# Performance work log

Hardware: AMD Instinct MI355X
Metric: run time of the kernel (lower is better)

Reference implementation:

```python
import jax, jax.numpy as jnp
import numpy as np

H_DIM = 256
N_HEADS = 8
HEAD_DIM = H_DIM // N_HEADS
B, N = 2, 2048
LN_EPS = 1e-5


def setup_inputs() -> dict:
    key = jax.random.key(0)
    ks = jax.random.split(key, 20)
    s = 1.0 / np.sqrt(H_DIM)
    inp = {
        'hidden': jax.random.normal(ks[0], (B, N, H_DIM), jnp.float32),
        'adjacency': jax.random.uniform(ks[1], (B, N, N), jnp.float32),
        'positions': jax.random.uniform(ks[2], (B, N, 2), jnp.float32),
        # linear weights stored as (in, out): y = x @ W + b
        'wq': jax.random.normal(ks[3], (H_DIM, H_DIM), jnp.float32) * s,
        'bq': jnp.zeros((H_DIM,), jnp.float32),
        'wk': jax.random.normal(ks[4], (H_DIM, H_DIM), jnp.float32) * s,
        'bk': jnp.zeros((H_DIM,), jnp.float32),
        'wv': jax.random.normal(ks[5], (H_DIM, H_DIM), jnp.float32) * s,
        'bv': jnp.zeros((H_DIM,), jnp.float32),
        'wo': jax.random.normal(ks[6], (H_DIM, H_DIM), jnp.float32) * s,
        'bo': jnp.zeros((H_DIM,), jnp.float32),
        'g1': jnp.ones((H_DIM,), jnp.float32),
        'b1': jnp.zeros((H_DIM,), jnp.float32),
        'g2': jnp.ones((H_DIM,), jnp.float32),
        'b2': jnp.zeros((H_DIM,), jnp.float32),
        'w_ff1': jax.random.normal(ks[7], (H_DIM, 4 * H_DIM), jnp.float32) * s,
        'b_ff1': jnp.zeros((4 * H_DIM,), jnp.float32),
        'w_ff2': jax.random.normal(ks[8], (4 * H_DIM, H_DIM), jnp.float32) * (1.0 / np.sqrt(4 * H_DIM)),
        'b_ff2': jnp.zeros((H_DIM,), jnp.float32),
    }
    return inp


def _layernorm(x, g, b):
    mu = jnp.mean(x, axis=-1, keepdims=True)
    var = jnp.var(x, axis=-1, keepdims=True)
    return (x - mu) * jax.lax.rsqrt(var + LN_EPS) * g + b


def reference(hidden, adjacency, positions, wq, bq, wk, bk, wv, bv, wo, bo,
              g1, b1, g2, b2, w_ff1, b_ff1, w_ff2, b_ff2):
    b_, n_, _ = hidden.shape
    normalized = _layernorm(hidden, g1, b1)
    # project and split heads: [B, H, N, Dh]
    def heads(x):
        return x.reshape(b_, n_, N_HEADS, HEAD_DIM).transpose(0, 2, 1, 3)
    q = heads(normalized @ wq + bq)
    k = heads(normalized @ wk + bk)
    v = heads(normalized @ wv + bv)
    logits = jnp.einsum('bhnd,bhmd->bhnm', q, k) / np.sqrt(HEAD_DIM)
    cond = adjacency[:, None, :, :]  # mode == 'connectivity'
    logits = logits + (2.0 * cond - 1.0)
    weights = jax.nn.softmax(logits, axis=-1)
    weights = weights * (0.25 + 0.75 * cond)
    weights = weights / jnp.maximum(weights.sum(axis=-1, keepdims=True), 1e-6)
    attended = jnp.einsum('bhnm,bhmd->bhnd', weights, v)
    attended = attended.transpose(0, 2, 1, 3).reshape(b_, n_, H_DIM)
    hidden = hidden + attended @ wo + bo
    h2 = _layernorm(hidden, g2, b2)
    ff = jax.nn.gelu(h2 @ w_ff1 + b_ff1, approximate=False) @ w_ff2 + b_ff2
    return hidden + ff
```

## Files before the change

### kernel.cpp

```cpp
#include <hip/hip_runtime.h>
#include <math.h>

#define BB 2
#define NN 2048
#define HD 256
#define NH 8
#define DH 32
#define NTOK (BB*NN)
#define QKVLD 768
#define NSPLIT 4

typedef _Float16 h8 __attribute__((ext_vector_type(8)));
typedef _Float16 h4 __attribute__((ext_vector_type(4)));
typedef float fx4 __attribute__((ext_vector_type(4)));

#define LOG2E 1.4426950408889634f
#define SQ_LOG2 0.25503486f

__global__ __launch_bounds__(256) void ln_kernel(const float* __restrict__ x,
    const float* __restrict__ g, const float* __restrict__ bta,
    _Float16* __restrict__ yh)
{
  int row  = blockIdx.x * 4 + (threadIdx.x >> 6);
  int lane = threadIdx.x & 63;
  const float* xr = x + (size_t)row * HD + lane * 4;
  float4 v = *(const float4*)xr;
  float s = v.x + v.y + v.z + v.w;
  #pragma unroll
  for (int off = 32; off > 0; off >>= 1) s += __shfl_xor(s, off);
  float mu = s * (1.0f / HD);
  float dx0 = v.x - mu, dx1 = v.y - mu, dx2 = v.z - mu, dx3 = v.w - mu;
  float ss = dx0*dx0 + dx1*dx1 + dx2*dx2 + dx3*dx3;
  #pragma unroll
  for (int off = 32; off > 0; off >>= 1) ss += __shfl_xor(ss, off);
  float rinv = rsqrtf(ss * (1.0f / HD) + 1e-5f);
  float4 gv = *(const float4*)(g   + lane * 4);
  float4 bv = *(const float4*)(bta + lane * 4);
  float o[4];
  o[0] = dx0 * rinv * gv.x + bv.x;
  o[1] = dx1 * rinv * gv.y + bv.y;
  o[2] = dx2 * rinv * gv.z + bv.z;
  o[3] = dx3 * rinv * gv.w + bv.w;
  h4 hh;
  #pragma unroll
  for (int j = 0; j < 4; j++) hh[j] = (_Float16)o[j];
  *(h4*)(yh + (size_t)row * HD + lane * 4) = hh;
}

__device__ __forceinline__ void do_transpose(const float* __restrict__ W,
    _Float16* __restrict__ Wh, int Nw, int rowoff, int ldout, float scale,
    int bx, int by, float (*tile)[33])
{
  int k0 = by * 32, n0 = bx * 32;
  int c = threadIdx.x & 31, r = threadIdx.x >> 5;
  #pragma unroll
  for (int i = 0; i < 4; i++)
    tile[r + i * 8][c] = W[(size_t)(k0 + r + i * 8) * Nw + n0 + c];
  __syncthreads();
  #pragma unroll
  for (int i = 0; i < 4; i++) {
    int n = r + i * 8;
    Wh[(size_t)(rowoff + n0 + n) * ldout + k0 + c] = (_Float16)(tile[c][n] * scale);
  }
}

__global__ __launch_bounds__(256) void prep_kernel(
    const float* wq, const float* wk, const float* wv, const float* wo,
    const float* wf1, const float* wf2,
    const float* bq, const float* bk, const float* bv,
    _Float16* WtQKVh, _Float16* WtOh, _Float16* WtF1h, _Float16* WtF2h,
    float* biasqkv)
{
  __shared__ float tile[32][33];
  int bid = blockIdx.x;
  if (bid < 64)        do_transpose(wq,  WtQKVh,  256,   0,  256, SQ_LOG2, bid & 7, bid >> 3, tile);
  else if (bid < 128)  do_transpose(wk,  WtQKVh,  256, 256,  256, 1.0f, (bid-64) & 7, (bid-64) >> 3, tile);
  else if (bid < 192)  do_transpose(wv,  WtQKVh,  256, 512,  256, 1.0f, (bid-128) & 7, (bid-128) >> 3, tile);
  else if (bid < 256)  do_transpose(wo,  WtOh,    256,   0,  256, 1.0f, (bid-192) & 7, (bid-192) >> 3, tile);
  else if (bid < 512)  do_transpose(wf1, WtF1h,  1024,   0,  256, 1.0f, (bid-256) & 31, (bid-256) >> 5, tile);
  else if (bid < 768)  do_transpose(wf2, WtF2h,   256,   0, 1024, 1.0f, (bid-512) & 7, (bid-512) >> 3, tile);
  else {
    #pragma unroll
    for (int j = 0; j < 3; j++) {
      int t = j * 256 + threadIdx.x;
      biasqkv[t] = (t < 256) ? bq[t] * SQ_LOG2 : (t < 512) ? bk[t - 256] : bv[t - 512];
    }
  }
}

template<int KK, int NT, int NX, int ACT, int RES, int OM>
__global__ __launch_bounds__(256) void gemm16_kernel(
    const _Float16* __restrict__ Ah, const _Float16* __restrict__ Wh,
    const float* __restrict__ bias, const float* __restrict__ resid,
    float* __restrict__ Cf, _Float16* __restrict__ Ch,
    _Float16* __restrict__ vtb, int N)
{
  const int lin = blockIdx.x;
  const int qch = gridDim.x >> 3;
  const int wg = (lin & 7) * qch + (lin >> 3);
  const int bx = wg % NX, by = wg / NX;
  const int n0 = bx * (NT * 16);
  const int m0 = by * 64;
  const int t = threadIdx.x, w = t >> 6, l = t & 63;
  const int ml = l & 15, g = l >> 4;
  const int mrow = m0 + w * 16 + ml;

  const _Float16* aph = Ah + (size_t)mrow * KK + g * 8;
  const _Float16* whp[NT];
  #pragma unroll
  for (int nt = 0; nt < NT; nt++)
    whp[nt] = Wh + (size_t)(n0 + nt * 16 + ml) * KK + g * 8;

  fx4 acc[NT];
  #pragma unroll
  for (int nt = 0; nt < NT; nt++) acc[nt] = (fx4){0.f, 0.f, 0.f, 0.f};

  #pragma unroll 4
  for (int k0 = 0; k0 < KK; k0 += 32) {
    h8 ah = *(const h8*)(aph + k0);
    #pragma unroll
    for (int nt = 0; nt < NT; nt++) {
      h8 wh = *(const h8*)(whp[nt] + k0);
      acc[nt] = __builtin_amdgcn_mfma_f32_16x16x32_f16(ah, wh, acc[nt], 0, 0, 0);
    }
  }

  #pragma unroll
  for (int nt = 0; nt < NT; nt++) {
    int n = n0 + nt * 16 + ml;
    float bv = bias[n];
    #pragma unroll
    for (int i = 0; i < 4; i++) {
      int m = m0 + w * 16 + 4 * g + i;
      float vv = acc[nt][i] + bv;
      if (ACT == 1) vv = 0.5f * vv * (1.0f + erff(vv * 0.70710678118654752f));
      if (RES)      vv += resid[(size_t)m * N + n];
      if (OM == 0) {
        Cf[(size_t)m * N + n] = vv;
      } else if (OM == 1) {
        Ch[(size_t)m * N + n] = (_Float16)vv;
      } else {
        if (n < 512) Ch[(size_t)m * QKVLD + n] = (_Float16)vv;
        else {
          int dim = n - 512, kv = m & (NN - 1), bb = m >> 11;
          int kvp = (kv & ~31) | ((kv & 15) << 1) | ((kv >> 4) & 1);
          vtb[((size_t)(bb * HD + dim)) * NN + kvp] = (_Float16)vv;
        }
      }
    }
  }
}

__global__ __launch_bounds__(256) void attn_mfma_kernel(
    const _Float16* __restrict__ qkv16, const _Float16* __restrict__ vtb,
    const float* __restrict__ adj,
    float* __restrict__ Opart, float* __restrict__ Mpart, float* __restrict__ Spart)
{
  __shared__ _Float16 Ksh[64][40];
  __shared__ _Float16 Vp[32][72];

  const int z = blockIdx.z;
  const int b = z >> 2, quarter = z & 3;
  const int h = blockIdx.y;
  const int q0 = blockIdx.x * 64;
  const int t = threadIdx.x;
  const int w = t >> 6, l = t & 63;
  const int m = l & 15, g = l >> 4;
  const int kvbase = quarter * (NN / NSPLIT);

  const int qrow = q0 + w * 16 + m;
  h8 qh = *(const h8*)(qkv16 + ((size_t)(b * NN + qrow)) * QKVLD + h * DH + g * 8);

  fx4 ot0 = {0.f, 0.f, 0.f, 0.f};
  fx4 ot1 = {0.f, 0.f, 0.f, 0.f};
  float M = -3.0e38f, S = 0.0f;

  const float* adjrow = adj + ((size_t)(b * NN + qrow)) * NN + kvbase;

  const int krow = t >> 2, kd0 = (t & 3) * 8;
  const int vdim = t >> 3, vkc = (t & 7) * 8;
  const _Float16* kbase = qkv16 + ((size_t)(b * NN + kvbase + krow)) * QKVLD + 256 + h * DH + kd0;
  const _Float16* vbase = vtb + ((size_t)(b * HD + h * DH + vdim)) * NN + kvbase + vkc;
  h8 kreg = *(const h8*)kbase;
  h8 vreg = *(const h8*)vbase;
  float4 adjreg[4];
  #pragma unroll
  for (int p = 0; p < 4; p++) adjreg[p] = *(const float4*)(adjrow + p * 16 + g * 4);

  for (int kt = 0; kt < NN / NSPLIT; kt += 64) {
    __syncthreads();
    *(h8*)&Ksh[krow][kd0] = kreg;
    *(h8*)&Vp[vdim][vkc]  = vreg;
    __syncthreads();

    float4 a4[4];
    #pragma unroll
    for (int p = 0; p < 4; p++) a4[p] = adjreg[p];
    if (kt + 64 < NN / NSPLIT) {
      kreg = *(const h8*)(kbase + (size_t)(kt + 64) * QKVLD);
      vreg = *(const h8*)(vbase + kt + 64);
      #pragma unroll
      for (int p = 0; p < 4; p++) adjreg[p] = *(const float4*)(adjrow + kt + 64 + p * 16 + g * 4);
    }

    h8 kh0 = *(const h8*)&Ksh[     m][g * 8];
    h8 kh1 = *(const h8*)&Ksh[16 + m][g * 8];
    h8 kh2 = *(const h8*)&Ksh[32 + m][g * 8];
    h8 kh3 = *(const h8*)&Ksh[48 + m][g * 8];
    fx4 z4 = {0.f, 0.f, 0.f, 0.f};
    fx4 st[4];
    st[0] = __builtin_amdgcn_mfma_f32_16x16x32_f16(kh0, qh, z4, 0, 0, 0);
    st[1] = __builtin_amdgcn_mfma_f32_16x16x32_f16(kh1, qh, z4, 0, 0, 0);
    st[2] = __builtin_amdgcn_mfma_f32_16x16x32_f16(kh2, qh, z4, 0, 0, 0);
    st[3] = __builtin_amdgcn_mfma_f32_16x16x32_f16(kh3, qh, z4, 0, 0, 0);

    float lv[16];
    float tmax = -3.0e38f;
    #pragma unroll
    for (int p = 0; p < 4; p++) {
      const float* ap = (const float*)&a4[p];
      #pragma unroll
      for (int i = 0; i < 4; i++) {
        float lvv = st[p][i] + (2.0f * LOG2E) * ap[i] - LOG2E;
        lv[p * 4 + i] = lvv;
        tmax = fmaxf(tmax, lvv);
      }
    }
    tmax = fmaxf(tmax, __shfl_xor(tmax, 16));
    tmax = fmaxf(tmax, __shfl_xor(tmax, 32));
    if (!__all(tmax <= M + 8.0f)) {
      float mnew = fmaxf(M, tmax);
      float resc = __builtin_amdgcn_exp2f(M - mnew);
      S *= resc; ot0 *= resc; ot1 *= resc;
      M = mnew;
    }
    float pv[16];
    #pragma unroll
    for (int p = 0; p < 4; p++) {
      const float* ap = (const float*)&a4[p];
      #pragma unroll
      for (int i = 0; i < 4; i++) {
        float e = __builtin_amdgcn_exp2f(lv[p * 4 + i] - M);
        float pp = (0.25f + 0.75f * ap[i]) * e;
        pv[p * 4 + i] = pp;
        S += pp;
      }
    }
    h8 ph0, ph1;
    #pragma unroll
    for (int q2 = 0; q2 < 4; q2++) {
      ph0[2*q2]     = (_Float16)pv[q2];
      ph0[2*q2 + 1] = (_Float16)pv[4 + q2];
      ph1[2*q2]     = (_Float16)pv[8 + q2];
      ph1[2*q2 + 1] = (_Float16)pv[12 + q2];
    }

    h8 v00 = *(const h8*)&Vp[m][g * 8];
    h8 v01 = *(const h8*)&Vp[m][32 + g * 8];
    h8 v10 = *(const h8*)&Vp[16 + m][g * 8];
    h8 v11 = *(const h8*)&Vp[16 + m][32 + g * 8];
    ot0 = __builtin_amdgcn_mfma_f32_16x16x32_f16(v00, ph0, ot0, 0, 0, 0);
    ot0 = __builtin_amdgcn_mfma_f32_16x16x32_f16(v01, ph1, ot0, 0, 0, 0);
    ot1 = __builtin_amdgcn_mfma_f32_16x16x32_f16(v10, ph0, ot1, 0, 0, 0);
    ot1 = __builtin_amdgcn_mfma_f32_16x16x32_f16(v11, ph1, ot1, 0, 0, 0);
  }

  S += __shfl_xor(S, 16);
  S += __shfl_xor(S, 32);

  size_t prow = ((size_t)(z * NH + h)) * NN + qrow;
  float* po = Opart + prow * 32;
  *(float4*)(po + 4 * g)      = make_float4(ot0[0], ot0[1], ot0[2], ot0[3]);
  *(float4*)(po + 16 + 4 * g) = make_float4(ot1[0], ot1[1], ot1[2], ot1[3]);
  if (g == 0) { Mpart[prow] = M; Spart[prow] = S; }
}

__global__ __launch_bounds__(256) void attn_combine_kernel(
    const float* __restrict__ Opart, const float* __restrict__ Mpart,
    const float* __restrict__ Spart, _Float16* __restrict__ atth)
{
  int idx = blockIdx.x * 256 + threadIdx.x;
  int dg  = idx & 7;
  int rowid = idx >> 3;
  int qrow = rowid & (NN - 1);
  int bh = rowid >> 11;
  int b = bh >> 3, h = bh & 7;
  size_t p[NSPLIT];
  float mz[NSPLIT], sz[NSPLIT];
  float mm = -3.0e38f;
  #pragma unroll
  for (int zq = 0; zq < NSPLIT; zq++) {
    p[zq] = ((size_t)((b * NSPLIT + zq) * NH + h)) * NN + qrow;
    mz[zq] = Mpart[p[zq]];
    sz[zq] = Spart[p[zq]];
    mm = fmaxf(mm, mz[zq]);
  }
  float den = 0.f;
  float ez[NSPLIT];
  #pragma unroll
  for (int zq = 0; zq < NSPLIT; zq++) {
    ez[zq] = __builtin_amdgcn_exp2f(mz[zq] - mm);
    den += sz[zq] * ez[zq];
  }
  float is = 1.0f / den;
  float ov[4] = {0.f, 0.f, 0.f, 0.f};
  #pragma unroll
  for (int zq = 0; zq < NSPLIT; zq++) {
    float4 o = *(const float4*)(Opart + p[zq] * 32 + dg * 4);
    ov[0] += o.x * ez[zq]; ov[1] += o.y * ez[zq];
    ov[2] += o.z * ez[zq]; ov[3] += o.w * ez[zq];
  }
  h4 hh;
  #pragma unroll
  for (int j = 0; j < 4; j++) hh[j] = (_Float16)(ov[j] * is);
  *(h4*)(atth + ((size_t)(b * NN + qrow)) * HD + h * DH + dg * 4) = hh;
}

extern "C" void kernel_launch(void* const* d_in, const int* in_sizes, int n_in,
                              void* d_out, int out_size, void* d_ws, size_t ws_size,
                              hipStream_t stream)
{
  const float* hidden    = (const float*)d_in[0];
  const float* adjacency = (const float*)d_in[1];
  const float* wq  = (const float*)d_in[3];
  const float* bq  = (const float*)d_in[4];
  const float* wk  = (const float*)d_in[5];
  const float* bk  = (const float*)d_in[6];
  const float* wv  = (const float*)d_in[7];
  const float* bv  = (const float*)d_in[8];
  const float* wo  = (const float*)d_in[9];
  const float* bo  = (const float*)d_in[10];
  const float* g1  = (const float*)d_in[11];
  const float* b1  = (const float*)d_in[12];
  const float* g2  = (const float*)d_in[13];
  const float* b2  = (const float*)d_in[14];
  const float* wf1 = (const float*)d_in[15];
  const float* bf1 = (const float*)d_in[16];
  const float* wf2 = (const float*)d_in[17];
  const float* bf2 = (const float*)d_in[18];
  float* out = (float*)d_out;

  char* base = (char*)d_ws;
  const size_t MB = 1024 * 1024;
  _Float16* norm1h = (_Float16*)(base);
  _Float16* qkv16  = (_Float16*)(base + 4*MB);
  _Float16* vtb    = (_Float16*)(base + 10*MB);
  _Float16* atth   = (_Float16*)(base + 12*MB);
  float*    hid2   = (float*)(base + 16*MB);
  float* Opart = (float*)(base + 20*MB);
  _Float16* ffah = (_Float16*)(base + 20*MB);
  float* Mpart = (float*)(base + 36*MB);
  float* Spart = (float*)(base + 36*MB + 512*1024);
  _Float16* wtb = (_Float16*)(base + 37*MB);
  _Float16* WtQKVh = wtb; wtb += 768 * 256;
  _Float16* WtOh   = wtb; wtb += 256 * 256;
  _Float16* WtF1h  = wtb; wtb += 1024 * 256;
  _Float16* WtF2h  = wtb; wtb += 256 * 1024;
  float* biasqkv = (float*)(base + 40*MB);

  prep_kernel<<<769, 256, 0, stream>>>(wq, wk, wv, wo, wf1, wf2, bq, bk, bv,
      WtQKVh, WtOh, WtF1h, WtF2h, biasqkv);

  ln_kernel<<<NTOK / 4, 256, 0, stream>>>(hidden, g1, b1, norm1h);

  gemm16_kernel<256, 4, 12, 0, 0, 2><<<768, 256, 0, stream>>>(
      norm1h, WtQKVh, biasqkv, nullptr, nullptr, qkv16, vtb, QKVLD);

  attn_mfma_kernel<<<dim3(NN / 64, NH, BB * NSPLIT), 256, 0, stream>>>(
      qkv16, vtb, adjacency, Opart, Mpart, Spart);
  attn_combine_kernel<<<(BB * NH * NN * 8) / 256, 256, 0, stream>>>(
      Opart, Mpart, Spart, atth);

  gemm16_kernel<256, 2, 8, 0, 1, 0><<<512, 256, 0, stream>>>(
      atth, WtOh, bo, hidden, hid2, nullptr, nullptr, 256);

  ln_kernel<<<NTOK / 4, 256, 0, stream>>>(hid2, g2, b2, norm1h);

  gemm16_kernel<256, 4, 16, 1, 0, 1><<<1024, 256, 0, stream>>>(
      norm1h, WtF1h, bf1, nullptr, nullptr, ffah, nullptr, 1024);

  gemm16_kernel<1024, 2, 8, 0, 1, 0><<<512, 256, 0, stream>>>(
      ffah, WtF2h, bf2, hid2, out, nullptr, nullptr, 256);
}
```

Measured before the change: 133.4 us.

## Double-buffer attention K/V tiles and store normalized fp16 partial outputs

The attention kernel now keeps two LDS buffers for K and V and writes the next tile after the current tile's MFMAs, so each iteration needs one barrier instead of two. The row-max reduction is restructured to shuffle only when a rescale is needed. Each split's partial output is normalized by its own sum and stored as fp16, which halves partial-output traffic, and the combine kernel reweights by S·exp. This adds LDS use and a small fp16 precision loss on the partials.

After: 132.0 us. Within noise of the previous version (-1.0%).

```diff
diff --git a/kernel.cpp b/kernel.cpp
--- a/kernel.cpp
+++ b/kernel.cpp
@@ -154,10 +154,10 @@
 __global__ __launch_bounds__(256) void attn_mfma_kernel(
     const _Float16* __restrict__ qkv16, const _Float16* __restrict__ vtb,
     const float* __restrict__ adj,
-    float* __restrict__ Opart, float* __restrict__ Mpart, float* __restrict__ Spart)
-{
-  __shared__ _Float16 Ksh[64][40];
-  __shared__ _Float16 Vp[32][72];
+    _Float16* __restrict__ Opart, float* __restrict__ Mpart, float* __restrict__ Spart)
+{
+  __shared__ _Float16 Ksh[2][64][40];
+  __shared__ _Float16 Vp[2][32][72];
 
   const int z = blockIdx.z;
   const int b = z >> 2, quarter = z & 3;
@@ -167,6 +167,7 @@
   const int w = t >> 6, l = t & 63;
   const int m = l & 15, g = l >> 4;
   const int kvbase = quarter * (NN / NSPLIT);
+  const int NTILES = NN / NSPLIT / 64;
 
   const int qrow = q0 + w * 16 + m;
   h8 qh = *(const h8*)(qkv16 + ((size_t)(b * NN + qrow)) * QKVLD + h * DH + g * 8);
@@ -181,32 +182,34 @@
   const int vdim = t >> 3, vkc = (t & 7) * 8;
   const _Float16* kbase = qkv16 + ((size_t)(b * NN + kvbase + krow)) * QKVLD + 256 + h * DH + kd0;
   const _Float16* vbase = vtb + ((size_t)(b * HD + h * DH + vdim)) * NN + kvbase + vkc;
+
   h8 kreg = *(const h8*)kbase;
   h8 vreg = *(const h8*)vbase;
   float4 adjreg[4];
   #pragma unroll
   for (int p = 0; p < 4; p++) adjreg[p] = *(const float4*)(adjrow + p * 16 + g * 4);
 
-  for (int kt = 0; kt < NN / NSPLIT; kt += 64) {
-    __syncthreads();
-    *(h8*)&Ksh[krow][kd0] = kreg;
-    *(h8*)&Vp[vdim][vkc]  = vreg;
-    __syncthreads();
-
+  *(h8*)&Ksh[0][krow][kd0] = kreg;
+  *(h8*)&Vp[0][vdim][vkc]  = vreg;
+  kreg = *(const h8*)(kbase + (size_t)64 * QKVLD);
+  vreg = *(const h8*)(vbase + 64);
+  __syncthreads();
+
+  for (int tt = 0; tt < NTILES; ++tt) {
+    const int cur = tt & 1;
     float4 a4[4];
     #pragma unroll
     for (int p = 0; p < 4; p++) a4[p] = adjreg[p];
-    if (kt + 64 < NN / NSPLIT) {
-      kreg = *(const h8*)(kbase + (size_t)(kt + 64) * QKVLD);
-      vreg = *(const h8*)(vbase + kt + 64);
+    if (tt + 1 < NTILES) {
       #pragma unroll
-      for (int p = 0; p < 4; p++) adjreg[p] = *(const float4*)(adjrow + kt + 64 + p * 16 + g * 4);
-    }
-
-    h8 kh0 = *(const h8*)&Ksh[     m][g * 8];
-    h8 kh1 = *(const h8*)&Ksh[16 + m][g * 8];
-    h8 kh2 = *(const h8*)&Ksh[32 + m][g * 8];
-    h8 kh3 = *(const h8*)&Ksh[48 + m][g * 8];
+      for (int p = 0; p < 4; p++)
+        adjreg[p] = *(const float4*)(adjrow + (tt + 1) * 64 + p * 16 + g * 4);
+    }
+
+    h8 kh0 = *(const h8*)&Ksh[cur][     m][g * 8];
+    h8 kh1 = *(const h8*)&Ksh[cur][16 + m][g * 8];
+    h8 kh2 = *(const h8*)&Ksh[cur][32 + m][g * 8];
+    h8 kh3 = *(const h8*)&Ksh[cur][48 + m][g * 8];
     fx4 z4 = {0.f, 0.f, 0.f, 0.f};
     fx4 st[4];
     st[0] = __builtin_amdgcn_mfma_f32_16x16x32_f16(kh0, qh, z4, 0, 0, 0);
@@ -215,26 +218,28 @@
     st[3] = __builtin_amdgcn_mfma_f32_16x16x32_f16(kh3, qh, z4, 0, 0, 0);
 
     float lv[16];
-    float tmax = -3.0e38f;
     #pragma unroll
     for (int p = 0; p < 4; p++) {
       const float* ap = (const float*)&a4[p];
       #pragma unroll
-      for (int i = 0; i < 4; i++) {
-        float lvv = st[p][i] + (2.0f * LOG2E) * ap[i] - LOG2E;
-        lv[p * 4 + i] = lvv;
-        tmax = fmaxf(tmax, lvv);
-      }
-    }
-    tmax = fmaxf(tmax, __shfl_xor(tmax, 16));
-    tmax = fmaxf(tmax, __shfl_xor(tmax, 32));
-    if (!__all(tmax <= M + 8.0f)) {
-      float mnew = fmaxf(M, tmax);
+      for (int i = 0; i < 4; i++)
+        lv[p * 4 + i] = st[p][i] + (2.0f * LOG2E) * ap[i] - LOG2E;
+    }
+    float x8[8];
+    #pragma unroll
+    for (int i = 0; i < 8; i++) x8[i] = fmaxf(lv[i], lv[i + 8]);
+    float x4[4];
+    #pragma unroll
+    for (int i = 0; i < 4; i++) x4[i] = fmaxf(x8[i], x8[i + 4]);
+    float lmax = fmaxf(fmaxf(x4[0], x4[1]), fmaxf(x4[2], x4[3]));
+    if (!__all(lmax <= M + 8.0f)) {
+      float rmax = fmaxf(lmax, __shfl_xor(lmax, 16));
+      rmax = fmaxf(rmax, __shfl_xor(rmax, 32));
+      float mnew = fmaxf(M, rmax);
       float resc = __builtin_amdgcn_exp2f(M - mnew);
       S *= resc; ot0 *= resc; ot1 *= resc;
       M = mnew;
     }
-    float pv[16];
     #pragma unroll
     for (int p = 0; p < 4; p++) {
       const float* ap = (const float*)&a4[p];
@@ -242,41 +247,58 @@
       for (int i = 0; i < 4; i++) {
         float e = __builtin_amdgcn_exp2f(lv[p * 4 + i] - M);
         float pp = (0.25f + 0.75f * ap[i]) * e;
-        pv[p * 4 + i] = pp;
+        lv[p * 4 + i] = pp;
         S += pp;
       }
     }
     h8 ph0, ph1;
     #pragma unroll
     for (int q2 = 0; q2 < 4; q2++) {
-      ph0[2*q2]     = (_Float16)pv[q2];
-      ph0[2*q2 + 1] = (_Float16)pv[4 + q2];
-      ph1[2*q2]     = (_Float16)pv[8 + q2];
-      ph1[2*q2 + 1] = (_Float16)pv[12 + q2];
-    }
-
-    h8 v00 = *(const h8*)&Vp[m][g * 8];
-    h8 v01 = *(const h8*)&Vp[m][32 + g * 8];
-    h8 v10 = *(const h8*)&Vp[16 + m][g * 8];
-    h8 v11 = *(const h8*)&Vp[16 + m][32 + g * 8];
+      ph0[2*q2]     = (_Float16)lv[q2];
+      ph0[2*q2 + 1] = (_Float16)lv[4 + q2];
+      ph1[2*q2]     = (_Float16)lv[8 + q2];
+      ph1[2*q2 + 1] = (_Float16)lv[12 + q2];
+    }
+
+    h8 v00 = *(const h8*)&Vp[cur][m][g * 8];
+    h8 v01 = *(const h8*)&Vp[cur][m][32 + g * 8];
+    h8 v10 = *(const h8*)&Vp[cur][16 + m][g * 8];
+    h8 v11 = *(const h8*)&Vp[cur][16 + m][32 + g * 8];
     ot0 = __builtin_amdgcn_mfma_f32_16x16x32_f16(v00, ph0, ot0, 0, 0, 0);
     ot0 = __builtin_amdgcn_mfma_f32_16x16x32_f16(v01, ph1, ot0, 0, 0, 0);
     ot1 = __builtin_amdgcn_mfma_f32_16x16x32_f16(v10, ph0, ot1, 0, 0, 0);
     ot1 = __builtin_amdgcn_mfma_f32_16x16x32_f16(v11, ph1, ot1, 0, 0, 0);
+
+    if (tt + 1 < NTILES) {
+      *(h8*)&Ksh[cur ^ 1][krow][kd0] = kreg;
+      *(h8*)&Vp[cur ^ 1][vdim][vkc]  = vreg;
+      if (tt + 2 < NTILES) {
+        kreg = *(const h8*)(kbase + (size_t)((tt + 2) * 64) * QKVLD);
+        vreg = *(const h8*)(vbase + (tt + 2) * 64);
+      }
+    }
+    __syncthreads();
   }
 
   S += __shfl_xor(S, 16);
   S += __shfl_xor(S, 32);
 
+  float is = 1.0f / S;
   size_t prow = ((size_t)(z * NH + h)) * NN + qrow;
-  float* po = Opart + prow * 32;
-  *(float4*)(po + 4 * g)      = make_float4(ot0[0], ot0[1], ot0[2], ot0[3]);
-  *(float4*)(po + 16 + 4 * g) = make_float4(ot1[0], ot1[1], ot1[2], ot1[3]);
+  _Float16* po = Opart + prow * 32;
+  h4 o0h, o1h;
+  #pragma unroll
+  for (int j = 0; j < 4; j++) {
+    o0h[j] = (_Float16)(ot0[j] * is);
+    o1h[j] = (_Float16)(ot1[j] * is);
+  }
+  *(h4*)(po + 4 * g)      = o0h;
+  *(h4*)(po + 16 + 4 * g) = o1h;
   if (g == 0) { Mpart[prow] = M; Spart[prow] = S; }
 }
 
 __global__ __launch_bounds__(256) void attn_combine_kernel(
-    const float* __restrict__ Opart, const float* __restrict__ Mpart,
+    const _Float16* __restrict__ Opart, const float* __restrict__ Mpart,
     const float* __restrict__ Spart, _Float16* __restrict__ atth)
 {
   int idx = blockIdx.x * 256 + threadIdx.x;
@@ -296,23 +318,24 @@
     mm = fmaxf(mm, mz[zq]);
   }
   float den = 0.f;
-  float ez[NSPLIT];
+  float wz[NSPLIT];
   #pragma unroll
   for (int zq = 0; zq < NSPLIT; zq++) {
-    ez[zq] = __builtin_amdgcn_exp2f(mz[zq] - mm);
-    den += sz[zq] * ez[zq];
+    wz[zq] = sz[zq] * __builtin_amdgcn_exp2f(mz[zq] - mm);
+    den += wz[zq];
   }
   float is = 1.0f / den;
   float ov[4] = {0.f, 0.f, 0.f, 0.f};
   #pragma unroll
   for (int zq = 0; zq < NSPLIT; zq++) {
-    float4 o = *(const float4*)(Opart + p[zq] * 32 + dg * 4);
-    ov[0] += o.x * ez[zq]; ov[1] += o.y * ez[zq];
-    ov[2] += o.z * ez[zq]; ov[3] += o.w * ez[zq];
+    h4 o = *(const h4*)(Opart + p[zq] * 32 + dg * 4);
+    float wzz = wz[zq] * is;
+    #pragma unroll
+    for (int j = 0; j < 4; j++) ov[j] += wzz * (float)o[j];
   }
   h4 hh;
   #pragma unroll
-  for (int j = 0; j < 4; j++) hh[j] = (_Float16)(ov[j] * is);
+  for (int j = 0; j < 4; j++) hh[j] = (_Float16)ov[j];
   *(h4*)(atth + ((size_t)(b * NN + qrow)) * HD + h * DH + dg * 4) = hh;
 }
 
@@ -347,8 +370,8 @@
   _Float16* vtb    = (_Float16*)(base + 10*MB);
   _Float16* atth   = (_Float16*)(base + 12*MB);
   float*    hid2   = (float*)(base + 16*MB);
-  float* Opart = (float*)(base + 20*MB);
-  _Float16* ffah = (_Float16*)(base + 20*MB);
+  _Float16* Opart = (_Float16*)(base + 20*MB);
+  _Float16* ffah  = (_Float16*)(base + 20*MB);
   float* Mpart = (float*)(base + 36*MB);
   float* Spart = (float*)(base + 36*MB + 512*1024);
   _Float16* wtb = (_Float16*)(base + 37*MB);
```
